# Performance work log

Measured on AMD Instinct MI355X. Metric: run time of the kernel, lower is better.

The kernel has to match this reference:

```python
import jax, jax.numpy as jnp
import numpy as np

L = 4          # num_layers
DIM = 256      # model dim
HEADS = 8
DH = DIM // HEADS
WINDOW = 512   # sliding window size
FF = 4 * DIM
EPS = 1e-5


def setup_inputs() -> dict:
    key = jax.random.key(0)
    ks = jax.random.split(key, 13)
    B, S = 1, 4096
    s = 0.02
    inp = {
        "x": jax.random.normal(ks[0], (B, S, DIM), jnp.float32),
        # per-layer stacked weights (leading axis = layer) for lax.scan
        "wq": jax.random.normal(ks[1], (L, DIM, DIM), jnp.float32) * s,
        "bq": jnp.zeros((L, DIM), jnp.float32),
        "wk": jax.random.normal(ks[2], (L, DIM, DIM), jnp.float32) * s,
        "bk": jnp.zeros((L, DIM), jnp.float32),
        "wv": jax.random.normal(ks[3], (L, DIM, DIM), jnp.float32) * s,
        "bv": jnp.zeros((L, DIM), jnp.float32),
        "wo": jax.random.normal(ks[4], (L, DIM, DIM), jnp.float32) * s,
        "bo": jnp.zeros((L, DIM), jnp.float32),
        "w1": jax.random.normal(ks[5], (L, DIM, FF), jnp.float32) * s,
        "b1": jnp.zeros((L, FF), jnp.float32),
        "w2": jax.random.normal(ks[6], (L, FF, DIM), jnp.float32) * s,
        "b2": jnp.zeros((L, DIM), jnp.float32),
    }
    return inp


def _ln(x):
    # LayerNorm with elementwise_affine=False
    m = jnp.mean(x, axis=-1, keepdims=True)
    v = jnp.var(x, axis=-1, keepdims=True)
    return (x - m) / jnp.sqrt(v + EPS)


def reference(x, wq, bq, wk, bk, wv, bv, wo, bo, w1, b1, w2, b2):
    B, S, D = x.shape
    idx = jnp.arange(S)
    # sliding window mask: |q_idx - kv_idx| <= window_size // 2
    mask = jnp.abs(idx[:, None] - idx[None, :]) <= (WINDOW // 2)  # [S, S]
    neg = jnp.finfo(x.dtype).min
    scale = 1.0 / np.sqrt(DH)

    def layer(h, p):
        lwq, lbq, lwk, lbk, lwv, lbv, lwo, lbo, lw1, lb1, lw2, lb2 = p
        # pre-norm self-attention residual
        n = _ln(h)
        q = (n @ lwq + lbq).reshape(B, S, HEADS, DH)
        k = (n @ lwk + lbk).reshape(B, S, HEADS, DH)
        v = (n @ lwv + lbv).reshape(B, S, HEADS, DH)
        scores = jnp.einsum('bqhd,bkhd->bhqk', q, k) * scale
        scores = jnp.where(mask, scores, neg)
        attn = jax.nn.softmax(scores, axis=-1)
        o = jnp.einsum('bhqk,bkhd->bqhd', attn, v).reshape(B, S, D)
        h = h + o @ lwo + lbo
        # post-norm dense residual: x = norm(x); x = x + ffn(x)
        h = _ln(h)
        h = h + jax.nn.gelu(h @ lw1 + lb1) @ lw2 + lb2
        return h, None

    x, _ = jax.lax.scan(layer, x, (wq, bq, wk, bk, wv, bv, wo, bo, w1, b1, w2, b2))
    return x
```

## Files before the change

### kernel.cpp

```cpp
#include <hip/hip_runtime.h>
#include <math.h>

#define SEQ 4096
#define DIM 256
#define NH 8
#define DHD 32
#define FFD 1024
#define NLAYER 4

typedef unsigned short ushort_t;
typedef __attribute__((ext_vector_type(8))) short bf16x8;
typedef __attribute__((ext_vector_type(4))) float f32x4;

__device__ __forceinline__ float gelu_f(float x){
  const float c = 0.7978845608028654f;
  float x3 = x*x*x;
  return 0.5f * x * (1.0f + tanhf(c*(x + 0.044715f*x3)));
}

__device__ __forceinline__ ushort_t f2b(float f){
  union { float f; unsigned u; } x; x.f = f;
  unsigned r = x.u + 0x7FFF + ((x.u >> 16) & 1);
  return (ushort_t)(r >> 16);
}

__device__ __forceinline__ void gload16(void* lds, const void* g){
  __builtin_amdgcn_global_load_lds((const __attribute__((address_space(1))) void*)g,
                                   (__attribute__((address_space(3))) void*)lds, 16, 0, 0);
}

__device__ __forceinline__ int xcd_swz(int b, int nwg){
  return (b & 7)*(nwg >> 3) + (b >> 3);
}

__global__ __launch_bounds__(256) void wconv_kernel(
    const float* __restrict__ wq, const float* __restrict__ wk,
    const float* __restrict__ wv, const float* __restrict__ wo,
    const float* __restrict__ w1, const float* __restrict__ w2,
    ushort_t* __restrict__ wt){
  __shared__ ushort_t tile[64][65];
  int b = blockIdx.x, tid = threadIdx.x;
  const float* src; ushort_t* dst; int K, N, tk, tn;
  if (b < 256){
    int m = b>>6, rem = b&63, l = rem>>4, t = rem&15;
    K = 256; N = 256; tk = t>>2; tn = t&3;
    const float* s4 = (m==0)?wq:(m==1)?wk:(m==2)?wv:wo;
    src = s4 + (size_t)l*65536;
    dst = wt + (size_t)(m*NLAYER + l)*65536;
  } else if (b < 512){
    int rem = b-256, l = rem>>6, t = rem&63;
    K = 256; N = 1024; tk = t>>4; tn = t&15;
    src = w1 + (size_t)l*262144;
    dst = wt + 1048576 + (size_t)l*262144;
  } else {
    int rem = b-512, l = rem>>6, t = rem&63;
    K = 1024; N = 256; tk = t>>2; tn = t&3;
    src = w2 + (size_t)l*262144;
    dst = wt + 2097152 + (size_t)l*262144;
  }
  int k0 = tk*64, n0 = tn*64;
  #pragma unroll
  for (int i=0;i<16;i++){
    int idx = tid + 256*i, row = idx>>6, col = idx&63;
    tile[row][col] = f2b(src[(size_t)(k0+row)*N + n0+col]);
  }
  __syncthreads();
  #pragma unroll
  for (int i=0;i<16;i++){
    int idx = tid + 256*i, nrow = idx>>6, kcol = idx&63;
    dst[(size_t)(n0+nrow)*K + k0+kcol] = tile[kcol][nrow];
  }
}

__global__ __launch_bounds__(256) void gemm_kernel(
    const ushort_t* __restrict__ A, const ushort_t* __restrict__ Wt,
    const float* __restrict__ bias, const float* __restrict__ R,
    float* __restrict__ Cf, ushort_t* __restrict__ Cb,
    int M, int N, int K, int act){
  __shared__ ushort_t As[32*256];
  __shared__ ushort_t Bs[64*256];
  int tid = threadIdx.x;
  int w = tid>>6, lane = tid&63;
  int wr = w>>1, wc = w&1;
  int q4 = lane>>4, u = lane&15;
  int fid = xcd_swz(blockIdx.y*4 + blockIdx.x, 512);
  int m0 = (fid>>2)*32, n0 = (fid&3)*64;
  f32x4 acc[2];
  acc[0] = (f32x4){0.f,0.f,0.f,0.f};
  acc[1] = (f32x4){0.f,0.f,0.f,0.f};

  for (int k0 = 0; k0 < K; k0 += 256){
    if (k0) __syncthreads();
    #pragma unroll
    for (int i=0;i<4;i++){
      int idx = tid + 256*i;
      int row = idx>>5, ch = idx&31;
      gload16(&As[idx*8], &A[(size_t)(m0+row)*K + k0 + ((ch^(row&7))*8)]);
    }
    #pragma unroll
    for (int i=0;i<8;i++){
      int idx = tid + 256*i;
      int row = idx>>5, ch = idx&31;
      gload16(&Bs[idx*8], &Wt[(size_t)(n0+row)*K + k0 + ((ch^(row&7))*8)]);
    }
    __syncthreads();
    #pragma unroll
    for (int kk=0;kk<8;kk++){
      int ar = wr*16 + u;
      bf16x8 af = *(const bf16x8*)&As[ar*256 + (((kk*4+q4)^(ar&7))*8)];
      #pragma unroll
      for (int j=0;j<2;j++){
        int br = wc*32 + j*16 + u;
        bf16x8 bf = *(const bf16x8*)&Bs[br*256 + (((kk*4+q4)^(br&7))*8)];
        acc[j] = __builtin_amdgcn_mfma_f32_16x16x32_bf16(af, bf, acc[j], 0, 0, 0);
      }
    }
  }
  #pragma unroll
  for (int j=0;j<2;j++){
    #pragma unroll
    for (int t=0;t<4;t++){
      int m = m0 + wr*16 + q4*4 + t;
      int n = n0 + wc*32 + j*16 + u;
      float val = acc[j][t] + bias[n];
      if (R)   val += R[(size_t)m*N + n];
      if (act) val = gelu_f(val);
      if (Cf)  Cf[(size_t)m*N + n] = val;
      if (Cb)  Cb[(size_t)m*N + n] = f2b(val);
    }
  }
}

__global__ __launch_bounds__(256) void ffn1ln_kernel(
    const float* __restrict__ h1, const ushort_t* __restrict__ Wt,
    const float* __restrict__ bias, ushort_t* __restrict__ Cb){
  __shared__ ushort_t As[32*256];
  __shared__ ushort_t Bs[64*256];
  int tid = threadIdx.x;
  int w = tid>>6, lane = tid&63;
  int wr = w>>1, wc = w&1;
  int q4 = lane>>4, u = lane&15;
  int fid = xcd_swz(blockIdx.y*16 + blockIdx.x, 512);
  int n0 = (fid & 15)*64;
  int mg = (fid >> 4);
  #pragma unroll
  for (int i=0;i<8;i++){
    int idx = tid + 256*i;
    int row = idx>>5, ch = idx&31;
    gload16(&Bs[idx*8], &Wt[(size_t)(n0+row)*DIM + ((ch^(row&7))*8)]);
  }
  for (int ms=0; ms<4; ms++){
    int m0 = mg*128 + ms*32;
    #pragma unroll
    for (int r=0;r<8;r++){
      int row = w*8 + r;
      float4 v = *(const float4*)&h1[(size_t)(m0+row)*DIM + lane*4];
      float s  = v.x+v.y+v.z+v.w;
      float sq = v.x*v.x+v.y*v.y+v.z*v.z+v.w*v.w;
      #pragma unroll
      for (int off=32; off>0; off>>=1){ s += __shfl_down(s,off); sq += __shfl_down(sq,off); }
      s = __shfl(s,0); sq = __shfl(sq,0);
      float mean = s*(1.0f/DIM), var = sq*(1.0f/DIM) - mean*mean;
      float rinv = rsqrtf(var + 1e-5f);
      int ch = lane>>1, half = lane&1;
      ushort4 o4;
      o4.x = f2b((v.x-mean)*rinv); o4.y = f2b((v.y-mean)*rinv);
      o4.z = f2b((v.z-mean)*rinv); o4.w = f2b((v.w-mean)*rinv);
      *(ushort4*)&As[row*256 + ((ch^(row&7))*8 + half*4)] = o4;
    }
    __syncthreads();
    f32x4 acc[2];
    acc[0]=(f32x4){0.f,0.f,0.f,0.f}; acc[1]=(f32x4){0.f,0.f,0.f,0.f};
    #pragma unroll
    for (int kk=0;kk<8;kk++){
      int ar = wr*16 + u;
      bf16x8 af = *(const bf16x8*)&As[ar*256 + (((kk*4+q4)^(ar&7))*8)];
      #pragma unroll
      for (int j=0;j<2;j++){
        int br = wc*32 + j*16 + u;
        bf16x8 bf = *(const bf16x8*)&Bs[br*256 + (((kk*4+q4)^(br&7))*8)];
        acc[j] = __builtin_amdgcn_mfma_f32_16x16x32_bf16(af, bf, acc[j], 0, 0, 0);
      }
    }
    #pragma unroll
    for (int j=0;j<2;j++)
      #pragma unroll
      for (int t=0;t<4;t++){
        int m = m0 + wr*16 + q4*4 + t;
        int n = n0 + wc*32 + j*16 + u;
        Cb[(size_t)m*FFD + n] = f2b(gelu_f(acc[j][t] + bias[n]));
      }
    if (ms < 3) __syncthreads();
  }
}

__global__ __launch_bounds__(256) void ffn2ln_kernel(
    const ushort_t* __restrict__ A, const ushort_t* __restrict__ Wt,
    const float* __restrict__ bias, const float* __restrict__ h1,
    float* __restrict__ Cf){
  __shared__ ushort_t As[32*256];
  __shared__ ushort_t Bs[64*256];
  __shared__ float lnm[32];
  __shared__ float lnr[32];
  const int K = FFD, N = DIM;
  int tid = threadIdx.x;
  int w = tid>>6, lane = tid&63;
  int wr = w>>1, wc = w&1;
  int q4 = lane>>4, u = lane&15;
  int fid = xcd_swz(blockIdx.y*4 + blockIdx.x, 512);
  int m0 = (fid>>2)*32, n0 = (fid&3)*64;
  f32x4 acc[2];
  acc[0] = (f32x4){0.f,0.f,0.f,0.f};
  acc[1] = (f32x4){0.f,0.f,0.f,0.f};

  for (int k0 = 0; k0 < K; k0 += 256){
    if (k0) __syncthreads();
    #pragma unroll
    for (int i=0;i<4;i++){
      int idx = tid + 256*i;
      int row = idx>>5, ch = idx&31;
      gload16(&As[idx*8], &A[(size_t)(m0+row)*K + k0 + ((ch^(row&7))*8)]);
    }
    #pragma unroll
    for (int i=0;i<8;i++){
      int idx = tid + 256*i;
      int row = idx>>5, ch = idx&31;
      gload16(&Bs[idx*8], &Wt[(size_t)(n0+row)*K + k0 + ((ch^(row&7))*8)]);
    }
    if (k0 == 0){
      #pragma unroll
      for (int r=0;r<8;r++){
        int row = w*8 + r;
        float4 v = *(const float4*)&h1[(size_t)(m0+row)*DIM + lane*4];
        float s  = v.x+v.y+v.z+v.w;
        float sq = v.x*v.x+v.y*v.y+v.z*v.z+v.w*v.w;
        #pragma unroll
        for (int off=32; off>0; off>>=1){ s += __shfl_down(s,off); sq += __shfl_down(sq,off); }
        s = __shfl(s,0); sq = __shfl(sq,0);
        float mean = s*(1.0f/DIM), var = sq*(1.0f/DIM) - mean*mean;
        float rinv = rsqrtf(var + 1e-5f);
        if (lane == 0){ lnm[row] = mean; lnr[row] = rinv; }
      }
    }
    __syncthreads();
    #pragma unroll
    for (int kk=0;kk<8;kk++){
      int ar = wr*16 + u;
      bf16x8 af = *(const bf16x8*)&As[ar*256 + (((kk*4+q4)^(ar&7))*8)];
      #pragma unroll
      for (int j=0;j<2;j++){
        int br = wc*32 + j*16 + u;
        bf16x8 bf = *(const bf16x8*)&Bs[br*256 + (((kk*4+q4)^(br&7))*8)];
        acc[j] = __builtin_amdgcn_mfma_f32_16x16x32_bf16(af, bf, acc[j], 0, 0, 0);
      }
    }
  }
  #pragma unroll
  for (int j=0;j<2;j++){
    #pragma unroll
    for (int t=0;t<4;t++){
      int m = m0 + wr*16 + q4*4 + t;
      int n = n0 + wc*32 + j*16 + u;
      float val = acc[j][t] + bias[n];
      val += (h1[(size_t)m*DIM + n] - lnm[m - m0]) * lnr[m - m0];
      Cf[(size_t)m*N + n] = val;
    }
  }
}

__global__ __launch_bounds__(256) void qkv_kernel(
    const float* __restrict__ hin,
    const ushort_t* __restrict__ wtq, const ushort_t* __restrict__ wtk, const ushort_t* __restrict__ wtv,
    const float* __restrict__ bqp, const float* __restrict__ bkp, const float* __restrict__ bvp,
    ushort_t* __restrict__ qo, ushort_t* __restrict__ ko, ushort_t* __restrict__ vo){
  __shared__ ushort_t As[32*256];
  __shared__ ushort_t Bs[64*256];
  int tid = threadIdx.x;
  int w = tid>>6, lane = tid&63;
  int wr = w>>1, wc = w&1;
  int q4 = lane>>4, u = lane&15;
  int fid = xcd_swz(blockIdx.y*4 + blockIdx.x, 512);
  int m0 = (fid>>2)*32, n0 = (fid&3)*64;

  #pragma unroll
  for (int i=0;i<8;i++){
    int idx = tid + 256*i;
    int row = idx>>5, ch = idx&31;
    gload16(&Bs[idx*8], &wtq[(size_t)(n0+row)*DIM + ((ch^(row&7))*8)]);
  }
  #pragma unroll
  for (int r=0;r<8;r++){
    int row = w*8 + r;
    float4 v = *(const float4*)&hin[(size_t)(m0+row)*DIM + lane*4];
    float s  = v.x+v.y+v.z+v.w;
    float sq = v.x*v.x+v.y*v.y+v.z*v.z+v.w*v.w;
    #pragma unroll
    for (int off=32; off>0; off>>=1){ s += __shfl_down(s,off); sq += __shfl_down(sq,off); }
    s = __shfl(s,0); sq = __shfl(sq,0);
    float mean = s*(1.0f/DIM), var = sq*(1.0f/DIM) - mean*mean;
    float rinv = rsqrtf(var + 1e-5f);
    int ch = lane>>1, half = lane&1;
    ushort4 o4;
    o4.x = f2b((v.x-mean)*rinv); o4.y = f2b((v.y-mean)*rinv);
    o4.z = f2b((v.z-mean)*rinv); o4.w = f2b((v.w-mean)*rinv);
    *(ushort4*)&As[row*256 + ((ch^(row&7))*8 + half*4)] = o4;
  }
  __syncthreads();

  #pragma unroll
  for (int z=0; z<3; z++){
    const float* bias = (z==0)?bqp:(z==1)?bkp:bvp;
    ushort_t* Cb      = (z==0)?qo :(z==1)?ko :vo;
    f32x4 acc[2];
    acc[0]=(f32x4){0.f,0.f,0.f,0.f}; acc[1]=(f32x4){0.f,0.f,0.f,0.f};
    #pragma unroll
    for (int kk=0;kk<8;kk++){
      int ar = wr*16 + u;
      bf16x8 af = *(const bf16x8*)&As[ar*256 + (((kk*4+q4)^(ar&7))*8)];
      #pragma unroll
      for (int j=0;j<2;j++){
        int br = wc*32 + j*16 + u;
        bf16x8 bf = *(const bf16x8*)&Bs[br*256 + (((kk*4+q4)^(br&7))*8)];
        acc[j] = __builtin_amdgcn_mfma_f32_16x16x32_bf16(af, bf, acc[j], 0, 0, 0);
      }
    }
    if (z < 2){
      __syncthreads();
      const ushort_t* Wn = (z==0)?wtk:wtv;
      #pragma unroll
      for (int i=0;i<8;i++){
        int idx = tid + 256*i;
        int row = idx>>5, ch = idx&31;
        gload16(&Bs[idx*8], &Wn[(size_t)(n0+row)*DIM + ((ch^(row&7))*8)]);
      }
    }
    #pragma unroll
    for (int j=0;j<2;j++)
      #pragma unroll
      for (int t=0;t<4;t++){
        int m = m0 + wr*16 + q4*4 + t;
        int n = n0 + wc*32 + j*16 + u;
        Cb[(size_t)m*DIM + n] = f2b(acc[j][t] + bias[n]);
      }
    if (z < 2) __syncthreads();
  }
}

__global__ __launch_bounds__(256) void attn_kernel(
    const ushort_t* __restrict__ q, const ushort_t* __restrict__ k,
    const ushort_t* __restrict__ v, ushort_t* __restrict__ out){
  int fid = xcd_swz(blockIdx.y*64 + blockIdx.x, 512);
  int q0 = (fid & 63) * 64;
  int h  = fid >> 6;
  int tid = threadIdx.x;
  int w = tid >> 6;
  int lane = tid & 63;
  int u = lane & 15, q4 = lane >> 4;

  __shared__ ushort_t Ks[2][64][40];
  __shared__ ushort_t Vt[2][32][72];
  __shared__ ushort_t Pw[4][16][72];

  bf16x8 aq = *(const bf16x8*)(q + (size_t)(q0 + w*16 + u)*DIM + h*DHD + q4*8);

  float m[4], l[4];
  f32x4 acc[2];
  #pragma unroll
  for (int t=0;t<4;t++){ m[t] = -INFINITY; l[t] = 0.f; }
  acc[0] = (f32x4){0.f,0.f,0.f,0.f};
  acc[1] = (f32x4){0.f,0.f,0.f,0.f};

  const float sl2 = 0.25510703448358519f;

  int lo = q0 - 256; if (lo < 0) lo = 0;
  int hi = q0 + 63 + 256; if (hi > SEQ-1) hi = SEQ-1;
  int kt0 = (lo >> 6) << 6;
  int kt1 = (hi >> 6) << 6;

  int key = tid >> 2, d0 = (tid & 3) * 8;
  int vd0 = w * 8;

  bf16x8 kr = *(const bf16x8*)(k + (size_t)(kt0+key)*DIM + h*DHD + d0);
  bf16x8 vr = *(const bf16x8*)(v + (size_t)(kt0+lane)*DIM + h*DHD + vd0);
  *(bf16x8*)&Ks[0][key][d0] = kr;
  #pragma unroll
  for (int j=0;j<8;j++) Vt[0][vd0+j][lane] = (ushort_t)vr[j];

  int p = 0;
  for (int kt = kt0; kt <= kt1; kt += 64, p ^= 1){
    __syncthreads();
    bool have_next = (kt + 64 <= kt1);
    if (have_next){
      kr = *(const bf16x8*)(k + (size_t)(kt+64+key)*DIM + h*DHD + d0);
      vr = *(const bf16x8*)(v + (size_t)(kt+64+lane)*DIM + h*DHD + vd0);
    }

    f32x4 sc[4];
    #pragma unroll
    for (int t4=0;t4<4;t4++){
      bf16x8 bk = *(const bf16x8*)&Ks[p][t4*16 + u][q4*8];
      sc[t4] = __builtin_amdgcn_mfma_f32_16x16x32_bf16(aq, bk, (f32x4){0.f,0.f,0.f,0.f}, 0, 0, 0);
    }

    bool needs_mask = (kt < q0-192) || (kt > q0+192);
    #pragma unroll
    for (int t=0;t<4;t++){
      float mx = -INFINITY;
      if (needs_mask){
        int q_idx = q0 + w*16 + q4*4 + t;
        #pragma unroll
        for (int t4=0;t4<4;t4++){
          float s = sc[t4][t] * sl2;
          int k_idx = kt + t4*16 + u;
          int diff = q_idx - k_idx; if (diff < 0) diff = -diff;
          if (diff > 256) s = -INFINITY;
          sc[t4][t] = s;
          mx = fmaxf(mx, s);
        }
      } else {
        #pragma unroll
        for (int t4=0;t4<4;t4++){
          float s = sc[t4][t] * sl2;
          sc[t4][t] = s;
          mx = fmaxf(mx, s);
        }
      }
      mx = fmaxf(mx, __shfl_xor(mx, 1));
      mx = fmaxf(mx, __shfl_xor(mx, 2));
      mx = fmaxf(mx, __shfl_xor(mx, 4));
      mx = fmaxf(mx, __shfl_xor(mx, 8));
      float nm = fmaxf(m[t], mx);
      float al = exp2f(m[t] - nm);
      float rs = 0.f;
      #pragma unroll
      for (int t4=0;t4<4;t4++){
        float pv = exp2f(sc[t4][t] - nm);
        rs += pv;
        Pw[w][q4*4+t][t4*16+u] = f2b(pv);
      }
      rs += __shfl_xor(rs, 1);
      rs += __shfl_xor(rs, 2);
      rs += __shfl_xor(rs, 4);
      rs += __shfl_xor(rs, 8);
      l[t] = l[t]*al + rs;
      m[t] = nm;
      acc[0][t] *= al;
      acc[1][t] *= al;
    }
    #pragma unroll
    for (int kk=0;kk<2;kk++){
      bf16x8 ap = *(const bf16x8*)&Pw[w][u][kk*32 + q4*8];
      #pragma unroll
      for (int d=0; d<2; d++){
        bf16x8 bvf = *(const bf16x8*)&Vt[p][d*16 + u][kk*32 + q4*8];
        acc[d] = __builtin_amdgcn_mfma_f32_16x16x32_bf16(ap, bvf, acc[d], 0, 0, 0);
      }
    }
    if (have_next){
      *(bf16x8*)&Ks[p^1][key][d0] = kr;
      #pragma unroll
      for (int j=0;j<8;j++) Vt[p^1][vd0+j][lane] = (ushort_t)vr[j];
    }
  }

  float rl[4];
  #pragma unroll
  for (int t=0;t<4;t++) rl[t] = 1.0f / l[t];
  #pragma unroll
  for (int d=0; d<2; d++)
    #pragma unroll
    for (int t=0;t<4;t++)
      out[(size_t)(q0 + w*16 + q4*4 + t)*DIM + h*DHD + d*16 + u] = f2b(acc[d][t]*rl[t]);
}

extern "C" void kernel_launch(void* const* d_in, const int* in_sizes, int n_in,
                              void* d_out, int out_size, void* d_ws, size_t ws_size,
                              hipStream_t stream) {
  const float* x  = (const float*)d_in[0];
  const float* wq = (const float*)d_in[1];
  const float* bq = (const float*)d_in[2];
  const float* wk = (const float*)d_in[3];
  const float* bk = (const float*)d_in[4];
  const float* wv = (const float*)d_in[5];
  const float* bv = (const float*)d_in[6];
  const float* wo = (const float*)d_in[7];
  const float* bo = (const float*)d_in[8];
  const float* w1 = (const float*)d_in[9];
  const float* b1 = (const float*)d_in[10];
  const float* w2 = (const float*)d_in[11];
  const float* b2 = (const float*)d_in[12];
  float* out = (float*)d_out;
  float* ws  = (float*)d_ws;

  ushort_t* wt    = (ushort_t*)ws;
  ushort_t* abuf  = (ushort_t*)(ws + 1572864);
  ushort_t* ffbf  = (ushort_t*)(ws + 2097152);
  float* qb = ws + 4194304;
  float* kb = ws + 5242880;
  float* vb = ws + 6291456;
  float* hb = ws + 7340032;
  ushort_t* qbh = (ushort_t*)qb;
  ushort_t* kbh = (ushort_t*)kb;
  ushort_t* vbh = (ushort_t*)vb;

  const ushort_t* w1t_base = wt + 1048576;
  const ushort_t* w2t_base = wt + 2097152;

  const dim3 blk(256);
  wconv_kernel<<<768, blk, 0, stream>>>(wq, wk, wv, wo, w1, w2, wt);

  for (int l = 0; l < NLAYER; l++){
    const float* hin = (l == 0) ? x : hb;
    const ushort_t* lwq = wt + (size_t)(0*NLAYER + l)*65536;
    const ushort_t* lwk = wt + (size_t)(1*NLAYER + l)*65536;
    const ushort_t* lwv = wt + (size_t)(2*NLAYER + l)*65536;
    const ushort_t* lwo = wt + (size_t)(3*NLAYER + l)*65536;
    const ushort_t* lw1 = w1t_base + (size_t)l*262144;
    const ushort_t* lw2 = w2t_base + (size_t)l*262144;

    qkv_kernel<<<dim3(4,128), blk, 0, stream>>>(hin, lwq, lwk, lwv,
        bq + (size_t)l*DIM, bk + (size_t)l*DIM, bv + (size_t)l*DIM, qbh, kbh, vbh);
    attn_kernel<<<dim3(SEQ/64, NH), blk, 0, stream>>>(qbh, kbh, vbh, abuf);
    gemm_kernel<<<dim3(4,128), blk, 0, stream>>>(abuf, lwo, bo + (size_t)l*DIM,
        hin, qb, nullptr, SEQ, DIM, DIM, 0);
    ffn1ln_kernel<<<dim3(16,32), blk, 0, stream>>>(qb, lw1, b1 + (size_t)l*FFD,
        ffbf);
    float* hout = (l == NLAYER-1) ? out : hb;
    ffn2ln_kernel<<<dim3(4,128), blk, 0, stream>>>(ffbf, lw2, b2 + (size_t)l*DIM,
        qb, hout);
  }
}
```

Baseline: 369.4 us.

## Process two 64-query tiles per attention block to reuse K/V tiles

Each attention workgroup now handles 128 queries as two 64-row halves that share each staged K/V tile in shared memory, halving the grid to 256 blocks. This is meant to cut redundant global K/V loads and LDS staging across overlapping sliding windows. In exchange it doubles per-thread accumulator state, which raises register pressure. It also lowers parallelism to 256 blocks on a large GPU, which may leave compute units idle.

```diff
diff --git a/kernel.cpp b/kernel.cpp
--- a/kernel.cpp
+++ b/kernel.cpp
@@ -349,9 +349,9 @@
 __global__ __launch_bounds__(256) void attn_kernel(
     const ushort_t* __restrict__ q, const ushort_t* __restrict__ k,
     const ushort_t* __restrict__ v, ushort_t* __restrict__ out){
-  int fid = xcd_swz(blockIdx.y*64 + blockIdx.x, 512);
-  int q0 = (fid & 63) * 64;
-  int h  = fid >> 6;
+  int fid = xcd_swz(blockIdx.y*32 + blockIdx.x, 256);
+  int q0 = (fid & 31) * 128;
+  int h  = fid >> 5;
   int tid = threadIdx.x;
   int w = tid >> 6;
   int lane = tid & 63;
@@ -361,21 +361,24 @@
   __shared__ ushort_t Vt[2][32][72];
   __shared__ ushort_t Pw[4][16][72];
 
-  bf16x8 aq = *(const bf16x8*)(q + (size_t)(q0 + w*16 + u)*DIM + h*DHD + q4*8);
-
-  float m[4], l[4];
-  f32x4 acc[2];
-  #pragma unroll
-  for (int t=0;t<4;t++){ m[t] = -INFINITY; l[t] = 0.f; }
-  acc[0] = (f32x4){0.f,0.f,0.f,0.f};
-  acc[1] = (f32x4){0.f,0.f,0.f,0.f};
+  bf16x8 aq0 = *(const bf16x8*)(q + (size_t)(q0 +      w*16 + u)*DIM + h*DHD + q4*8);
+  bf16x8 aq1 = *(const bf16x8*)(q + (size_t)(q0 + 64 + w*16 + u)*DIM + h*DHD + q4*8);
+
+  float m0_[4], l0_[4], m1_[4], l1_[4];
+  f32x4 acc0[2], acc1[2];
+  #pragma unroll
+  for (int t=0;t<4;t++){ m0_[t]=-INFINITY; l0_[t]=0.f; m1_[t]=-INFINITY; l1_[t]=0.f; }
+  acc0[0]=(f32x4){0.f,0.f,0.f,0.f}; acc0[1]=(f32x4){0.f,0.f,0.f,0.f};
+  acc1[0]=(f32x4){0.f,0.f,0.f,0.f}; acc1[1]=(f32x4){0.f,0.f,0.f,0.f};
 
   const float sl2 = 0.25510703448358519f;
 
-  int lo = q0 - 256; if (lo < 0) lo = 0;
-  int hi = q0 + 63 + 256; if (hi > SEQ-1) hi = SEQ-1;
+  int lo = q0 - 256;        if (lo < 0) lo = 0;
+  int hi = q0 + 127 + 256;  if (hi > SEQ-1) hi = SEQ-1;
   int kt0 = (lo >> 6) << 6;
   int kt1 = (hi >> 6) << 6;
+  int h0_hi = q0 + 63 + 256;  if (h0_hi > SEQ-1) h0_hi = SEQ-1;
+  int h1_lo = q0 + 64 - 256;  if (h1_lo < 0) h1_lo = 0;
 
   int key = tid >> 2, d0 = (tid & 3) * 8;
   int vd0 = w * 8;
@@ -395,67 +398,79 @@
       vr = *(const bf16x8*)(v + (size_t)(kt+64+lane)*DIM + h*DHD + vd0);
     }
 
-    f32x4 sc[4];
-    #pragma unroll
-    for (int t4=0;t4<4;t4++){
-      bf16x8 bk = *(const bf16x8*)&Ks[p][t4*16 + u][q4*8];
-      sc[t4] = __builtin_amdgcn_mfma_f32_16x16x32_bf16(aq, bk, (f32x4){0.f,0.f,0.f,0.f}, 0, 0, 0);
-    }
-
-    bool needs_mask = (kt < q0-192) || (kt > q0+192);
-    #pragma unroll
-    for (int t=0;t<4;t++){
-      float mx = -INFINITY;
-      if (needs_mask){
-        int q_idx = q0 + w*16 + q4*4 + t;
+    #pragma unroll
+    for (int half=0; half<2; half++){
+      if (half==0 && kt > h0_hi) continue;
+      if (half==1 && kt < h1_lo) continue;
+      int qb0 = q0 + half*64;
+      bf16x8 aq = half ? aq1 : aq0;
+      float*  mh = half ? m1_ : m0_;
+      float*  lh = half ? l1_ : l0_;
+      f32x4* ah = half ? acc1 : acc0;
+
+      f32x4 sc[4];
+      #pragma unroll
+      for (int t4=0;t4<4;t4++){
+        bf16x8 bk = *(const bf16x8*)&Ks[p][t4*16 + u][q4*8];
+        sc[t4] = __builtin_amdgcn_mfma_f32_16x16x32_bf16(aq, bk, (f32x4){0.f,0.f,0.f,0.f}, 0, 0, 0);
+      }
+
+      bool needs_mask = (kt < qb0-192) || (kt > qb0+192);
+      #pragma unroll
+      for (int t=0;t<4;t++){
+        float mx = -INFINITY;
+        if (needs_mask){
+          int q_idx = qb0 + w*16 + q4*4 + t;
+          #pragma unroll
+          for (int t4=0;t4<4;t4++){
+            float s = sc[t4][t] * sl2;
+            int k_idx = kt + t4*16 + u;
+            int diff = q_idx - k_idx; if (diff < 0) diff = -diff;
+            if (diff > 256) s = -INFINITY;
+            sc[t4][t] = s;
+            mx = fmaxf(mx, s);
+          }
+        } else {
+          #pragma unroll
+          for (int t4=0;t4<4;t4++){
+            float s = sc[t4][t] * sl2;
+            sc[t4][t] = s;
+            mx = fmaxf(mx, s);
+          }
+        }
+        mx = fmaxf(mx, __shfl_xor(mx, 1));
+        mx = fmaxf(mx, __shfl_xor(mx, 2));
+        mx = fmaxf(mx, __shfl_xor(mx, 4));
+        mx = fmaxf(mx, __shfl_xor(mx, 8));
+        float nm = fmaxf(mh[t], mx);
+        float al = exp2f(mh[t] - nm);
+        float rs = 0.f;
         #pragma unroll
         for (int t4=0;t4<4;t4++){
-          float s = sc[t4][t] * sl2;
-          int k_idx = kt + t4*16 + u;
-          int diff = q_idx - k_idx; if (diff < 0) diff = -diff;
-          if (diff > 256) s = -INFINITY;
-          sc[t4][t] = s;
-          mx = fmaxf(mx, s);
+          float pv = exp2f(sc[t4][t] - nm);
+          rs += pv;
+          Pw[w][q4*4+t][t4*16+u] = f2b(pv);
         }
-      } else {
+        rs += __shfl_xor(rs, 1);
+        rs += __shfl_xor(rs, 2);
+        rs += __shfl_xor(rs, 4);
+        rs += __shfl_xor(rs, 8);
+        lh[t] = lh[t]*al + rs;
+        mh[t] = nm;
+        ah[0][t] *= al;
+        ah[1][t] *= al;
+      }
+      #pragma unroll
+      for (int kk=0;kk<2;kk++){
+        bf16x8 ap = *(const bf16x8*)&Pw[w][u][kk*32 + q4*8];
         #pragma unroll
-        for (int t4=0;t4<4;t4++){
-          float s = sc[t4][t] * sl2;
-          sc[t4][t] = s;
-          mx = fmaxf(mx, s);
+        for (int d=0; d<2; d++){
+          bf16x8 bvf = *(const bf16x8*)&Vt[p][d*16 + u][kk*32 + q4*8];
+          ah[d] = __builtin_amdgcn_mfma_f32_16x16x32_bf16(ap, bvf, ah[d], 0, 0, 0);
         }
       }
-      mx = fmaxf(mx, __shfl_xor(mx, 1));
-      mx = fmaxf(mx, __shfl_xor(mx, 2));
-      mx = fmaxf(mx, __shfl_xor(mx, 4));
-      mx = fmaxf(mx, __shfl_xor(mx, 8));
-      float nm = fmaxf(m[t], mx);
-      float al = exp2f(m[t] - nm);
-      float rs = 0.f;
-      #pragma unroll
-      for (int t4=0;t4<4;t4++){
-        float pv = exp2f(sc[t4][t] - nm);
-        rs += pv;
-        Pw[w][q4*4+t][t4*16+u] = f2b(pv);
-      }
-      rs += __shfl_xor(rs, 1);
-      rs += __shfl_xor(rs, 2);
-      rs += __shfl_xor(rs, 4);
-      rs += __shfl_xor(rs, 8);
-      l[t] = l[t]*al + rs;
-      m[t] = nm;
-      acc[0][t] *= al;
-      acc[1][t] *= al;
-    }
-    #pragma unroll
-    for (int kk=0;kk<2;kk++){
-      bf16x8 ap = *(const bf16x8*)&Pw[w][u][kk*32 + q4*8];
-      #pragma unroll
-      for (int d=0; d<2; d++){
-        bf16x8 bvf = *(const bf16x8*)&Vt[p][d*16 + u][kk*32 + q4*8];
-        acc[d] = __builtin_amdgcn_mfma_f32_16x16x32_bf16(ap, bvf, acc[d], 0, 0, 0);
-      }
-    }
+    }
+
     if (have_next){
       *(bf16x8*)&Ks[p^1][key][d0] = kr;
       #pragma unroll
@@ -463,14 +478,13 @@
     }
   }
 
-  float rl[4];
-  #pragma unroll
-  for (int t=0;t<4;t++) rl[t] = 1.0f / l[t];
   #pragma unroll
   for (int d=0; d<2; d++)
     #pragma unroll
-    for (int t=0;t<4;t++)
-      out[(size_t)(q0 + w*16 + q4*4 + t)*DIM + h*DHD + d*16 + u] = f2b(acc[d][t]*rl[t]);
+    for (int t=0;t<4;t++){
+      out[(size_t)(q0 +      w*16 + q4*4 + t)*DIM + h*DHD + d*16 + u] = f2b(acc0[d][t]/l0_[t]);
+      out[(size_t)(q0 + 64 + w*16 + q4*4 + t)*DIM + h*DHD + d*16 + u] = f2b(acc1[d][t]/l1_[t]);
+    }
 }
 
 extern "C" void kernel_launch(void* const* d_in, const int* in_sizes, int n_in,
@@ -520,7 +534,7 @@
 
     qkv_kernel<<<dim3(4,128), blk, 0, stream>>>(hin, lwq, lwk, lwv,
         bq + (size_t)l*DIM, bk + (size_t)l*DIM, bv + (size_t)l*DIM, qbh, kbh, vbh);
-    attn_kernel<<<dim3(SEQ/64, NH), blk, 0, stream>>>(qbh, kbh, vbh, abuf);
+    attn_kernel<<<dim3(32, NH), blk, 0, stream>>>(qbh, kbh, vbh, abuf);
     gemm_kernel<<<dim3(4,128), blk, 0, stream>>>(abuf, lwo, bo + (size_t)l*DIM,
         hin, qb, nullptr, SEQ, DIM, DIM, 0);
     ffn1ln_kernel<<<dim3(16,32), blk, 0, stream>>>(qb, lw1, b1 + (size_t)l*FFD,
```

Result: slower. 419.0 us (+13.4%).
